# Performance work log

Hardware: AMD Instinct MI355X
Metric: run time of the kernel (lower is better)

The kernel has to match this reference:

```python
import jax, jax.numpy as jnp
import numpy as np

N_NODES = 10000
N_EDGES = 160000
HIDDEN = 512
N_LAYERS = 5


def setup_inputs() -> dict:
    key = jax.random.key(0)
    ks = jax.random.split(key, 12)
    return {
        "feat": jax.random.normal(ks[0], (N_NODES, HIDDEN), dtype=jnp.float32),
        "adj_row": jax.random.randint(ks[1], (N_EDGES,), 0, N_NODES, dtype=jnp.int32),
        "adj_col": jax.random.randint(ks[2], (N_EDGES,), 0, N_NODES, dtype=jnp.int32),
        "adj_val": jax.random.uniform(ks[3], (N_EDGES,), dtype=jnp.float32),
        "Wg": jax.random.normal(ks[4], (N_LAYERS, HIDDEN, HIDDEN), dtype=jnp.float32) * 0.02,
        "bg": jnp.zeros((N_LAYERS, HIDDEN), dtype=jnp.float32),
        "vw1": jax.random.normal(ks[5], (HIDDEN, HIDDEN), dtype=jnp.float32) * 0.02,
        "vb1": jnp.zeros((HIDDEN,), dtype=jnp.float32),
        "vw2": jax.random.normal(ks[6], (HIDDEN, 1), dtype=jnp.float32) * 0.02,
        "vb2": jnp.zeros((1,), dtype=jnp.float32),
    }


def _spmm(adj_row, adj_col, adj_val, x, n):
    # out[r] = sum_e adj_val[e] * x[adj_col[e]] for edges with adj_row[e] == r
    gathered = adj_val[:, None] * x[adj_col]  # [E, H]
    return jax.ops.segment_sum(gathered, adj_row, num_segments=n)


def reference(feat, adj_row, adj_col, adj_val, Wg, bg, vw1, vb1, vw2, vb2):
    n = feat.shape[0]
    x = feat
    for i in range(N_LAYERS):  # 5 structurally identical GraphConv layers
        h = x @ Wg[i]                                 # dense GEMM [N,H]
        agg = _spmm(adj_row, adj_col, adj_val, h, n)  # sparse aggregation
        x = jax.nn.relu(agg + bg[i])                  # bias + ReLU (dropout = eval identity)
    h = jax.nn.relu(x @ vw1 + vb1)
    return jax.nn.sigmoid(h @ vw2 + vb2)  # [N, 1]
```

## Files before the change

### kernel.cpp

```cpp
#include <hip/hip_runtime.h>

#define H 512
#define NNODES 10000
#define NEDGES 160000
#define NLAYERS 5

typedef __attribute__((ext_vector_type(8))) short short8;
typedef __attribute__((ext_vector_type(4))) float floatx4;

__device__ inline unsigned short f2bf(float v) {
    union { float f; unsigned int u; } x; x.f = v;
    unsigned int r = (x.u + 0x7fffu + ((x.u >> 16) & 1u)) >> 16;
    return (unsigned short)r;
}
__device__ inline float bf2f(unsigned short u) {
    union { unsigned int u; float f; } x; x.u = ((unsigned int)u) << 16; return x.f;
}
__device__ inline void gl_lds16(const void* g, void* l) {
    __builtin_amdgcn_global_load_lds((const __attribute__((address_space(1))) void*)g,
                                     (__attribute__((address_space(3))) void*)l, 16, 0, 0);
}

__global__ void zero_int(int* __restrict__ p, int n) {
    int i = blockIdx.x * blockDim.x + threadIdx.x;
    if (i < n) p[i] = 0;
}

__global__ void cvt_f32_bf16(const float* __restrict__ in, unsigned short* __restrict__ out, int n4) {
    int i = blockIdx.x * blockDim.x + threadIdx.x;
    if (i < n4) {
        float4 v = ((const float4*)in)[i];
        ushort4 o;
        o.x = f2bf(v.x); o.y = f2bf(v.y); o.z = f2bf(v.z); o.w = f2bf(v.w);
        ((ushort4*)out)[i] = o;
    }
}

__global__ void transpose_cvt6(const float* __restrict__ Wg, const float* __restrict__ vw1,
                               unsigned short* __restrict__ Wt) {
    __shared__ float tile[32][33];
    const int z = blockIdx.z;
    const float* in = (z < NLAYERS) ? (Wg + (size_t)z * H * H) : vw1;
    unsigned short* out = Wt + (size_t)z * H * H;
    const int bx = blockIdx.x * 32;
    const int by = blockIdx.y * 32;
    const int tx = threadIdx.x, ty = threadIdx.y;
    for (int i = ty; i < 32; i += 8)
        tile[i][tx] = in[(size_t)(by + i) * H + bx + tx];
    __syncthreads();
    for (int i = ty; i < 32; i += 8)
        out[(size_t)(bx + i) * H + by + tx] = f2bf(tile[tx][i]);
}

__global__ void edge_hist(const int* __restrict__ rows, int* __restrict__ counts, int n) {
    int i = blockIdx.x * blockDim.x + threadIdx.x;
    if (i < n) atomicAdd(&counts[rows[i]], 1);
}

__global__ __launch_bounds__(1024)
void scan_rows_pad(const int* __restrict__ counts, int* __restrict__ row_ptr, int n) {
    __shared__ int sums[1024];
    const int t = threadIdx.x;
    const int base = t * 16;
    int local[16];
    int s = 0;
#pragma unroll
    for (int i = 0; i < 16; ++i) {
        int idx = base + i;
        int v = (idx < n) ? ((counts[idx] + 7) & ~7) : 0;
        local[i] = s;
        s += v;
    }
    sums[t] = s;
    __syncthreads();
    for (int off = 1; off < 1024; off <<= 1) {
        int v = (t >= off) ? sums[t - off] : 0;
        __syncthreads();
        sums[t] += v;
        __syncthreads();
    }
    const int prefix = (t == 0) ? 0 : sums[t - 1];
#pragma unroll
    for (int i = 0; i < 16; ++i) {
        int idx = base + i;
        if (idx < n) row_ptr[idx] = prefix + local[i];
    }
    if (t == 0) row_ptr[n] = sums[1023];
}

__global__ void edge_scatter(const int* __restrict__ rows, const int* __restrict__ colsin,
                             const float* __restrict__ valsin, const int* __restrict__ row_ptr,
                             int* __restrict__ fill, int* __restrict__ colsout,
                             float* __restrict__ valsout, int n) {
    int i = blockIdx.x * blockDim.x + threadIdx.x;
    if (i < n) {
        int r = rows[i];
        int pos = row_ptr[r] + atomicAdd(&fill[r], 1);
        colsout[pos] = colsin[i];
        valsout[pos] = valsin[i];
    }
}

__device__ __forceinline__ void gemm_tile_body(
    const unsigned short* __restrict__ A, const unsigned short* __restrict__ Bt,
    unsigned short* __restrict__ C, const float* __restrict__ bias,
    int has_bias_relu, int M, int tileM, int tileN,
    unsigned short* lsA, unsigned short* lsB) {
    const int t = threadIdx.x;
    const int lane = t & 63;
    const int wave = t >> 6;
    const int wm = wave >> 1, wn = wave & 1;
    const int quad = lane >> 4, r16 = lane & 15;

    floatx4 acc[4][2] = {};

    const unsigned short* ap[4];
#pragma unroll
    for (int q = 0; q < 4; ++q) {
        const int c = t + 256 * q;
        const int row = c >> 3;
        int g = tileM + row; if (g >= M) g = M - 1;
        ap[q] = A + (size_t)g * 512 + (((c & 7) ^ (row & 7)) * 8);
    }
    const unsigned short* bp[2];
#pragma unroll
    for (int q = 0; q < 2; ++q) {
        const int c = t + 256 * q;
        const int row = c >> 3;
        bp[q] = Bt + (size_t)(tileN + row) * 512 + (((c & 7) ^ (row & 7)) * 8);
    }

    for (int k0 = 0; k0 < 512; k0 += 64) {
        gl_lds16(ap[0] + k0, lsA + (size_t)t * 8);
        gl_lds16(ap[1] + k0, lsA + (size_t)(t + 256) * 8);
        gl_lds16(ap[2] + k0, lsA + (size_t)(t + 512) * 8);
        gl_lds16(ap[3] + k0, lsA + (size_t)(t + 768) * 8);
        gl_lds16(bp[0] + k0, lsB + (size_t)t * 8);
        gl_lds16(bp[1] + k0, lsB + (size_t)(t + 256) * 8);
        __syncthreads();

        short8 af[4][2], bfr[2][2];
#pragma unroll
        for (int i = 0; i < 4; ++i) {
            const int row = wm * 64 + i * 16 + r16;
#pragma unroll
            for (int kk = 0; kk < 2; ++kk) {
                const int kcw = kk * 4 + quad;
                af[i][kk] = *(const short8*)&lsA[(size_t)(row * 8 + (kcw ^ (row & 7))) * 8];
            }
        }
#pragma unroll
        for (int j = 0; j < 2; ++j) {
            const int row = wn * 32 + j * 16 + r16;
#pragma unroll
            for (int kk = 0; kk < 2; ++kk) {
                const int kcw = kk * 4 + quad;
                bfr[j][kk] = *(const short8*)&lsB[(size_t)(row * 8 + (kcw ^ (row & 7))) * 8];
            }
        }
#pragma unroll
        for (int kk = 0; kk < 2; ++kk)
#pragma unroll
            for (int i = 0; i < 4; ++i)
#pragma unroll
                for (int j = 0; j < 2; ++j)
                    acc[i][j] = __builtin_amdgcn_mfma_f32_16x16x32_bf16(af[i][kk], bfr[j][kk], acc[i][j], 0, 0, 0);
        __syncthreads();
    }

#pragma unroll
    for (int i = 0; i < 4; ++i) {
#pragma unroll
        for (int j = 0; j < 2; ++j) {
            const int col = tileN + wn * 32 + j * 16 + r16;
#pragma unroll
            for (int reg = 0; reg < 4; ++reg) {
                const int row = tileM + wm * 64 + i * 16 + quad * 4 + reg;
                if (row < M) {
                    float v = acc[i][j][reg];
                    if (has_bias_relu) { v += bias[col]; v = fmaxf(v, 0.f); }
                    C[(size_t)row * 512 + col] = f2bf(v);
                }
            }
        }
    }
}

__global__ __launch_bounds__(256)
void gemm_bf16_xcd(const unsigned short* __restrict__ A, const unsigned short* __restrict__ Bt,
                   unsigned short* __restrict__ C, const float* __restrict__ bias,
                   int has_bias_relu, int M) {
    __shared__ __align__(16) unsigned short lsA[128 * 64];
    __shared__ __align__(16) unsigned short lsB[64 * 64];
    const int L = blockIdx.x;
    const int m_low = L & 7;
    const int rest = L >> 3;
    const int n = rest & 7;
    const int m_high = rest >> 3;
    const int m = m_high * 8 + m_low;
    gemm_tile_body(A, Bt, C, bias, has_bias_relu, M, m * 128, n * 64, lsA, lsB);
}

__global__ __launch_bounds__(256)
void spmm_pad(const int* __restrict__ prow, const int* __restrict__ cols,
              const float* __restrict__ vals, const unsigned short* __restrict__ hmat,
              const float* __restrict__ bias, unsigned short* __restrict__ xout) {
    const int wave = threadIdx.x >> 6, lane = threadIdx.x & 63;
    const int r = blockIdx.x * 4 + wave;
    if (r >= NNODES) return;
    const int s = prow[r], e = prow[r + 1];
    const int cb = lane * 8;
    float acc[8] = {0.f, 0.f, 0.f, 0.f, 0.f, 0.f, 0.f, 0.f};

    for (int i = s; i < e; i += 8) {
        int c[8]; float v[8]; short8 g[8];
#pragma unroll
        for (int u = 0; u < 8; ++u) { c[u] = cols[i + u]; v[u] = vals[i + u]; }
#pragma unroll
        for (int u = 0; u < 8; ++u) g[u] = *(const short8*)(hmat + (size_t)c[u] * H + cb);
#pragma unroll
        for (int u = 0; u < 8; ++u)
#pragma unroll
            for (int j = 0; j < 8; ++j) acc[j] += v[u] * bf2f((unsigned short)g[u][j]);
    }

    short8 o;
#pragma unroll
    for (int j = 0; j < 8; ++j)
        o[j] = (short)f2bf(fmaxf(acc[j] + bias[cb + j], 0.f));
    *(short8*)(xout + (size_t)r * H + cb) = o;
}

__global__ __launch_bounds__(256)
void final_head(const unsigned short* __restrict__ h2, const float* __restrict__ w2,
                const float* __restrict__ b2, float* __restrict__ out, int n) {
    const int wave = threadIdx.x >> 6, lane = threadIdx.x & 63;
    const int r = blockIdx.x * 4 + wave;
    if (r >= n) return;
    const unsigned short* hrow = h2 + (size_t)r * H;
    float acc = 0.f;
#pragma unroll
    for (int i = 0; i < 8; ++i) {
        const int c = lane * 8 + i;
        acc += bf2f(hrow[c]) * w2[c];
    }
#pragma unroll
    for (int off = 32; off >= 1; off >>= 1) acc += __shfl_xor(acc, off, 64);
    if (lane == 0) out[r] = 1.f / (1.f + expf(-(acc + b2[0])));
}

extern "C" void kernel_launch(void* const* d_in, const int* in_sizes, int n_in,
                              void* d_out, int out_size, void* d_ws, size_t ws_size,
                              hipStream_t stream) {
    (void)in_sizes; (void)n_in; (void)out_size; (void)ws_size;
    const float* feat   = (const float*)d_in[0];
    const int* adj_row  = (const int*)d_in[1];
    const int* adj_col  = (const int*)d_in[2];
    const float* adj_val= (const float*)d_in[3];
    const float* Wg     = (const float*)d_in[4];
    const float* bg     = (const float*)d_in[5];
    const float* vw1    = (const float*)d_in[6];
    const float* vb1    = (const float*)d_in[7];
    const float* vw2    = (const float*)d_in[8];
    const float* vb2    = (const float*)d_in[9];
    float* out = (float*)d_out;

    char* ws = (char*)d_ws;
    unsigned short* x  = (unsigned short*)(ws + 0);
    unsigned short* h  = (unsigned short*)(ws + 10240000);
    unsigned short* Wt = (unsigned short*)(ws + 20480000);
    int*   prow    = (int*)(ws + 23625728);
    int*   counts  = (int*)(ws + 23785792);
    int*   fill    = (int*)(ws + 23825792);
    int*   colsP   = (int*)(ws + 23865792);
    float* valsP   = (float*)(ws + 24825792);

    zero_int<<<(20000 + 255) / 256, 256, 0, stream>>>(counts, 20000);
    zero_int<<<(480000 + 255) / 256, 256, 0, stream>>>(colsP, 480000);
    cvt_f32_bf16<<<(NNODES * H / 4 + 255) / 256, 256, 0, stream>>>(feat, x, NNODES * H / 4);
    transpose_cvt6<<<dim3(16, 16, 6), dim3(32, 8), 0, stream>>>(Wg, vw1, Wt);
    edge_hist<<<(NEDGES + 255) / 256, 256, 0, stream>>>(adj_row, counts, NEDGES);
    scan_rows_pad<<<1, 1024, 0, stream>>>(counts, prow, NNODES);
    edge_scatter<<<(NEDGES + 255) / 256, 256, 0, stream>>>(adj_row, adj_col, adj_val,
                                                           prow, fill, colsP, valsP, NEDGES);

    for (int l = 0; l < NLAYERS; ++l) {
        gemm_bf16_xcd<<<640, 256, 0, stream>>>(x, Wt + (size_t)l * H * H, h, nullptr, 0, NNODES);
        spmm_pad<<<(NNODES + 3) / 4, 256, 0, stream>>>(prow, colsP, valsP, h, bg + (size_t)l * H, x);
    }
    gemm_bf16_xcd<<<640, 256, 0, stream>>>(x, Wt + (size_t)NLAYERS * H * H, h, vb1, 1, NNODES);
    final_head<<<(NNODES + 3) / 4, 256, 0, stream>>>(h, vw2, vb2, out, NNODES);
}
```

Baseline: 327.6 us.

## Double-buffer GEMM LDS tiles and prefetch SpMM indices with packed FMA

The GEMM k-loop now uses two LDS buffers, issuing the next k-slice's global-to-LDS loads before computing on the current one, so load latency can overlap MFMA work. LDS use per block doubles, which may reduce occupancy. The SpMM kernel software-prefetches the next chunk of column indices and values while the current gathers are in flight. It also unpacks bf16 pairs with bit ops and accumulates into float2 vectors so the compiler can emit packed FMAs.

```diff
diff --git a/kernel.cpp b/kernel.cpp
--- a/kernel.cpp
+++ b/kernel.cpp
@@ -7,6 +7,7 @@
 
 typedef __attribute__((ext_vector_type(8))) short short8;
 typedef __attribute__((ext_vector_type(4))) float floatx4;
+typedef __attribute__((ext_vector_type(2))) float floatx2;
 
 __device__ inline unsigned short f2bf(float v) {
     union { float f; unsigned int u; } x; x.f = v;
@@ -130,14 +131,26 @@
         bp[q] = Bt + (size_t)(tileN + row) * 512 + (((c & 7) ^ (row & 7)) * 8);
     }
 
-    for (int k0 = 0; k0 < 512; k0 += 64) {
-        gl_lds16(ap[0] + k0, lsA + (size_t)t * 8);
-        gl_lds16(ap[1] + k0, lsA + (size_t)(t + 256) * 8);
-        gl_lds16(ap[2] + k0, lsA + (size_t)(t + 512) * 8);
-        gl_lds16(ap[3] + k0, lsA + (size_t)(t + 768) * 8);
-        gl_lds16(bp[0] + k0, lsB + (size_t)t * 8);
-        gl_lds16(bp[1] + k0, lsB + (size_t)(t + 256) * 8);
-        __syncthreads();
+#define STAGE(buf, k0)                                                   \
+    do {                                                                 \
+        unsigned short* dA = lsA + (buf) * (128 * 64);                   \
+        unsigned short* dB = lsB + (buf) * (64 * 64);                    \
+        gl_lds16(ap[0] + (k0), dA + (size_t)t * 8);                      \
+        gl_lds16(ap[1] + (k0), dA + (size_t)(t + 256) * 8);              \
+        gl_lds16(ap[2] + (k0), dA + (size_t)(t + 512) * 8);              \
+        gl_lds16(ap[3] + (k0), dA + (size_t)(t + 768) * 8);              \
+        gl_lds16(bp[0] + (k0), dB + (size_t)t * 8);                      \
+        gl_lds16(bp[1] + (k0), dB + (size_t)(t + 256) * 8);              \
+    } while (0)
+
+    STAGE(0, 0);
+    __syncthreads();
+
+#pragma unroll
+    for (int it = 0; it < 8; ++it) {
+        if (it < 7) STAGE((it + 1) & 1, (it + 1) * 64);
+        const unsigned short* cA = lsA + (it & 1) * (128 * 64);
+        const unsigned short* cB = lsB + (it & 1) * (64 * 64);
 
         short8 af[4][2], bfr[2][2];
 #pragma unroll
@@ -146,7 +159,7 @@
 #pragma unroll
             for (int kk = 0; kk < 2; ++kk) {
                 const int kcw = kk * 4 + quad;
-                af[i][kk] = *(const short8*)&lsA[(size_t)(row * 8 + (kcw ^ (row & 7))) * 8];
+                af[i][kk] = *(const short8*)&cA[(size_t)(row * 8 + (kcw ^ (row & 7))) * 8];
             }
         }
 #pragma unroll
@@ -155,7 +168,7 @@
 #pragma unroll
             for (int kk = 0; kk < 2; ++kk) {
                 const int kcw = kk * 4 + quad;
-                bfr[j][kk] = *(const short8*)&lsB[(size_t)(row * 8 + (kcw ^ (row & 7))) * 8];
+                bfr[j][kk] = *(const short8*)&cB[(size_t)(row * 8 + (kcw ^ (row & 7))) * 8];
             }
         }
 #pragma unroll
@@ -167,6 +180,7 @@
                     acc[i][j] = __builtin_amdgcn_mfma_f32_16x16x32_bf16(af[i][kk], bfr[j][kk], acc[i][j], 0, 0, 0);
         __syncthreads();
     }
+#undef STAGE
 
 #pragma unroll
     for (int i = 0; i < 4; ++i) {
@@ -190,8 +204,8 @@
 void gemm_bf16_xcd(const unsigned short* __restrict__ A, const unsigned short* __restrict__ Bt,
                    unsigned short* __restrict__ C, const float* __restrict__ bias,
                    int has_bias_relu, int M) {
-    __shared__ __align__(16) unsigned short lsA[128 * 64];
-    __shared__ __align__(16) unsigned short lsB[64 * 64];
+    __shared__ __align__(16) unsigned short lsA[2 * 128 * 64];
+    __shared__ __align__(16) unsigned short lsB[2 * 64 * 64];
     const int L = blockIdx.x;
     const int m_low = L & 7;
     const int rest = L >> 3;
@@ -210,24 +224,48 @@
     if (r >= NNODES) return;
     const int s = prow[r], e = prow[r + 1];
     const int cb = lane * 8;
-    float acc[8] = {0.f, 0.f, 0.f, 0.f, 0.f, 0.f, 0.f, 0.f};
+    floatx2 acc2[4] = {};
+
+    int c[8]; float v[8];
+    if (s < e) {
+#pragma unroll
+        for (int u = 0; u < 8; ++u) { c[u] = cols[s + u]; v[u] = vals[s + u]; }
+    }
 
     for (int i = s; i < e; i += 8) {
-        int c[8]; float v[8]; short8 g[8];
-#pragma unroll
-        for (int u = 0; u < 8; ++u) { c[u] = cols[i + u]; v[u] = vals[i + u]; }
-#pragma unroll
-        for (int u = 0; u < 8; ++u) g[u] = *(const short8*)(hmat + (size_t)c[u] * H + cb);
-#pragma unroll
-        for (int u = 0; u < 8; ++u)
-#pragma unroll
-            for (int j = 0; j < 8; ++j) acc[j] += v[u] * bf2f((unsigned short)g[u][j]);
+        uint4 g[8];
+#pragma unroll
+        for (int u = 0; u < 8; ++u) g[u] = *(const uint4*)(hmat + (size_t)c[u] * H + cb);
+
+        const int nx = (i + 8 < e) ? (i + 8) : s;
+        int cn[8]; float vn[8];
+#pragma unroll
+        for (int u = 0; u < 8; ++u) { cn[u] = cols[nx + u]; vn[u] = vals[nx + u]; }
+
+#pragma unroll
+        for (int u = 0; u < 8; ++u) {
+            const floatx2 vv = {v[u], v[u]};
+            union { unsigned int u_; float f; } lo, hi;
+            floatx2 p;
+            lo.u_ = g[u].x << 16; hi.u_ = g[u].x & 0xffff0000u;
+            p[0] = lo.f; p[1] = hi.f; acc2[0] += vv * p;
+            lo.u_ = g[u].y << 16; hi.u_ = g[u].y & 0xffff0000u;
+            p[0] = lo.f; p[1] = hi.f; acc2[1] += vv * p;
+            lo.u_ = g[u].z << 16; hi.u_ = g[u].z & 0xffff0000u;
+            p[0] = lo.f; p[1] = hi.f; acc2[2] += vv * p;
+            lo.u_ = g[u].w << 16; hi.u_ = g[u].w & 0xffff0000u;
+            p[0] = lo.f; p[1] = hi.f; acc2[3] += vv * p;
+        }
+#pragma unroll
+        for (int u = 0; u < 8; ++u) { c[u] = cn[u]; v[u] = vn[u]; }
     }
 
     short8 o;
 #pragma unroll
-    for (int j = 0; j < 8; ++j)
-        o[j] = (short)f2bf(fmaxf(acc[j] + bias[cb + j], 0.f));
+    for (int k = 0; k < 4; ++k) {
+        o[2 * k]     = (short)f2bf(fmaxf(acc2[k][0] + bias[cb + 2 * k], 0.f));
+        o[2 * k + 1] = (short)f2bf(fmaxf(acc2[k][1] + bias[cb + 2 * k + 1], 0.f));
+    }
     *(short8*)(xout + (size_t)r * H + cb) = o;
 }
 
```

Result: slower. 336.2 us (+2.6%).
